# Kernel optimization log

Measured on AMD Instinct MI355X. Metric: run time of the kernel, lower is better.

Reference implementation:

```python
import jax, jax.numpy as jnp
import numpy as np

NV, NE, NI, D = 100000, 20000, 600000, 128

def setup_inputs() -> dict:
    key = jax.random.key(0)
    ks = jax.random.split(key, 16)
    inp = {
        'vfeat': jax.random.normal(ks[0], (NV, D), jnp.float32),
        'efeat': jax.random.normal(ks[1], (NE, D), jnp.float32),
        # positive regularization weights/sums (HNHN degree-based normalizers)
        'v_reg_weight': jax.random.uniform(ks[2], (NV, 1), jnp.float32, 0.5, 1.5),
        'v_reg_sum': jax.random.uniform(ks[3], (NV, 1), jnp.float32, 0.5, 1.5),
        'e_reg_weight': jax.random.uniform(ks[4], (NE, 1), jnp.float32, 0.5, 1.5),
        'e_reg_sum': jax.random.uniform(ks[5], (NE, 1), jnp.float32, 0.5, 1.5),
        'node_idx': jax.random.randint(ks[6], (NI,), 0, NV),
        'hedge_idx': jax.random.randint(ks[7], (NI,), 0, NE),
    }
    s = 1.0 / np.sqrt(D)
    inp['W1'] = jax.random.uniform(ks[8], (D, D), jnp.float32, -s, s)
    inp['b1'] = jax.random.uniform(ks[9], (D,), jnp.float32, -s, s)
    inp['Wve'] = jax.random.uniform(ks[10], (D, D), jnp.float32, -s, s)
    inp['bve'] = jax.random.uniform(ks[11], (D,), jnp.float32, -s, s)
    inp['Wev'] = jax.random.uniform(ks[12], (D, D), jnp.float32, -s, s)
    inp['bev'] = jax.random.uniform(ks[13], (D,), jnp.float32, -s, s)
    return inp


def reference(vfeat, efeat, v_reg_weight, v_reg_sum, e_reg_weight, e_reg_sum,
              node_idx, hedge_idx, W1, b1, Wve, bve, Wev, bev):
    # vertex projection (vtx_lin_1layer)
    feat_v = vfeat @ W1.T + b1                      # [NV, Dv]
    # node -> hyperedge pass ('in' etype)
    Wh_n = feat_v @ Wve.T + bve                     # [NV, De]
    w_in = v_reg_weight[node_idx] / e_reg_sum[hedge_idx]   # [NI, 1]
    feat_e = jax.ops.segment_sum(w_in * Wh_n[node_idx], hedge_idx,
                                 num_segments=NE)   # [NE, De]
    # hyperedge -> node pass ('con' etype)
    Wh_e = feat_e @ Wev.T + bev                     # [NE, Dv]
    w_con = e_reg_weight[hedge_idx] / v_reg_sum[node_idx]  # [NI, 1]
    feat_v_out = jax.ops.segment_sum(w_con * Wh_e[hedge_idx], node_idx,
                                     num_segments=NV)  # [NV, Dv]
    return feat_v_out
```

## Files before the change

### kernel.cpp

```cpp
#include <hip/hip_runtime.h>

#define D 128
#define GEMM_BLOCKS 512
#define PADE 16

typedef unsigned short ushort_t;
typedef short short8 __attribute__((ext_vector_type(8)));
typedef ushort_t ushort8v __attribute__((ext_vector_type(8)));
typedef float f32x4 __attribute__((ext_vector_type(4)));

static __device__ __forceinline__ unsigned short f2bf(float f){
  unsigned int b = __float_as_uint(f);
  unsigned int r = (b + 0x7FFFu + ((b >> 16) & 1u)) >> 16;
  return (unsigned short)r;
}
static __device__ __forceinline__ float bf2f(unsigned short u){
  return __uint_as_float(((unsigned int)u) << 16);
}


__global__ void k_wprep(const float* __restrict__ W1, const float* __restrict__ Wve,
                        const float* __restrict__ b1, const float* __restrict__ bve,
                        const float* __restrict__ Wev,
                        ushort_t* __restrict__ Wc, float* __restrict__ bc,
                        ushort_t* __restrict__ Wevb){
  int t = threadIdx.x;
  if (blockIdx.x < 128){
    int r = blockIdx.x;
    if (t < D){
      float acc = 0.f;
      for (int k = 0; k < D; ++k)
        acc += Wve[r * D + k] * W1[k * D + t];
      Wc[r * D + t] = f2bf(acc);
      if (t == 0){
        float s = 0.f;
        for (int k = 0; k < D; ++k) s += Wve[r * D + k] * b1[k];
        bc[r] = s + bve[r];
      }
    }
  } else {
    int i = (blockIdx.x - 128) * 256 + t;
    if (i < D * D) Wevb[i] = f2bf(Wev[i]);
  }
}


template<bool BF16IN>
__device__ __forceinline__ void gemm_body(const void* __restrict__ A_,
                                          const ushort_t* __restrict__ Wb,
                                          const float* __restrict__ bias,
                                          ushort_t* __restrict__ out, int M,
                                          int bid, int nblocks, ushort_t* Al){
  const int t = threadIdx.x;
  const int w = t >> 6;
  const int l = t & 63;
  const int l15 = l & 15;
  const int lh = l >> 4;

  short8 breg[4][8];
#pragma unroll
  for (int kc = 0; kc < 4; ++kc)
#pragma unroll
    for (int n0 = 0; n0 < 8; ++n0)
      breg[kc][n0] = *(const short8*)&Wb[(n0 * 16 + l15) * D + kc * 32 + lh * 8];

  float bias_r[8];
#pragma unroll
  for (int n0 = 0; n0 < 8; ++n0) bias_r[n0] = bias[n0 * 16 + l15];

  const int r_st = t >> 2;
  const int q_st = t & 3;
  const int ntile = (M + 63) >> 6;

  for (int tile = bid; tile < ntile; tile += nblocks){
    const int row0 = tile << 6;
    __syncthreads();
    {
      int r = row0 + r_st;
      ushort8v h[4];
      if (r < M){
        if (BF16IN){
          const ushort8v* src = (const ushort8v*)((const ushort_t*)A_ + (size_t)r * D + q_st * 32);
#pragma unroll
          for (int c = 0; c < 4; ++c) h[c] = src[c];
        } else {
          const float4* src = (const float4*)((const float*)A_ + (size_t)r * D + q_st * 32);
          float4 v[8];
#pragma unroll
          for (int i = 0; i < 8; ++i) v[i] = src[i];
#pragma unroll
          for (int c = 0; c < 4; ++c){
            h[c][0] = f2bf(v[2*c].x);   h[c][1] = f2bf(v[2*c].y);
            h[c][2] = f2bf(v[2*c].z);   h[c][3] = f2bf(v[2*c].w);
            h[c][4] = f2bf(v[2*c+1].x); h[c][5] = f2bf(v[2*c+1].y);
            h[c][6] = f2bf(v[2*c+1].z); h[c][7] = f2bf(v[2*c+1].w);
          }
        }
      } else {
#pragma unroll
        for (int c = 0; c < 4; ++c) h[c] = (ushort8v){0,0,0,0,0,0,0,0};
      }
#pragma unroll
      for (int c = 0; c < 4; ++c){
        int col = q_st * 32 + c * 8;
        int swz = col ^ ((r_st & 7) << 3);
        *(ushort8v*)&Al[r_st * D + swz] = h[c];
      }
    }
    __syncthreads();

    f32x4 acc[8];
#pragma unroll
    for (int n0 = 0; n0 < 8; ++n0) acc[n0] = (f32x4){0.f, 0.f, 0.f, 0.f};

#pragma unroll
    for (int kc = 0; kc < 4; ++kc){
      const int arow = w * 16 + l15;
      const int acol = (kc * 32 + lh * 8) ^ ((l15 & 7) << 3);
      short8 a = *(const short8*)&Al[arow * D + acol];
#pragma unroll
      for (int n0 = 0; n0 < 8; ++n0)
        acc[n0] = __builtin_amdgcn_mfma_f32_16x16x32_bf16(a, breg[kc][n0], acc[n0], 0, 0, 0);
    }

    const int rbase = row0 + w * 16 + lh * 4;
#pragma unroll
    for (int n0 = 0; n0 < 8; ++n0){
      const int colo = n0 * 16 + l15;
#pragma unroll
      for (int rg = 0; rg < 4; ++rg){
        int row = rbase + rg;
        if (row < M) out[(size_t)row * D + colo] = f2bf(acc[n0][rg] + bias_r[n0]);
      }
    }
  }
}

template<bool BF16IN>
__global__ __launch_bounds__(256, 2)
void k_gemm(const void* __restrict__ A_, const ushort_t* __restrict__ Wb,
            const float* __restrict__ bias, ushort_t* __restrict__ out, int M){
  __shared__ ushort_t Al[64 * D];
  gemm_body<BF16IN>(A_, Wb, bias, out, M, blockIdx.x, gridDim.x, Al);
}


__global__ __launch_bounds__(256, 2)
void k_ua(const float* __restrict__ A, const ushort_t* __restrict__ Wb,
          const float* __restrict__ bias, ushort_t* __restrict__ out, int M,
          const int* __restrict__ hedge_idx, int ni,
          int* __restrict__ cnt_e_pad, int* __restrict__ rank_e, int gb, int total){
  __shared__ ushort_t Al[64 * D];
  int i = blockIdx.x;
  long a0 = (long)i * gb / total, a1 = (long)(i + 1) * gb / total;
  if (a1 != a0){
    gemm_body<false>(A, Wb, bias, out, M, (int)a0, gb, Al);
  } else {
    int idx = (i - (int)a0) * 256 + threadIdx.x;
    if (idx < ni)
      rank_e[idx] = atomicAdd(&cnt_e_pad[hedge_idx[idx] * PADE], 1);
  }
}


template<int STRIDE>
__global__ void k_scan_partial(const int* __restrict__ cnt, int n, int* __restrict__ bsum){
  __shared__ int s[256];
  int b = blockIdx.x, t = threadIdx.x;
  int base = b * 1024;
  int acc = 0;
  for (int j = t; j < 1024; j += 256){
    int idx = base + j;
    if (idx < n) acc += cnt[(size_t)idx * STRIDE];
  }
  s[t] = acc; __syncthreads();
  for (int o = 128; o > 0; o >>= 1){
    if (t < o) s[t] += s[t + o];
    __syncthreads();
  }
  if (t == 0) bsum[b] = s[0];
}

__global__ void k_scan_bsums(int* __restrict__ bsum, int nb){
  __shared__ int s[256];
  int t = threadIdx.x;
  int runbase = 0;
  for (int base = 0; base < nb; base += 256){
    int v = (base + t < nb) ? bsum[base + t] : 0;
    s[t] = v;
    __syncthreads();
    for (int o = 1; o < 256; o <<= 1){
      int x = (t >= o) ? s[t - o] : 0;
      __syncthreads();
      s[t] += x;
      __syncthreads();
    }
    int total = s[255];
    if (base + t < nb) bsum[base + t] = runbase + (s[t] - v);
    __syncthreads();
    runbase += total;
  }
}

template<int STRIDE>
__global__ void k_scan_final(const int* __restrict__ cnt, int n,
                             const int* __restrict__ bsum, int* __restrict__ off,
                             int* __restrict__ cout){
  __shared__ int s[256];
  int b = blockIdx.x, t = threadIdx.x;
  int base = b * 1024 + t * 4;
  int v0 = (base + 0 < n) ? cnt[(size_t)(base + 0) * STRIDE] : 0;
  int v1 = (base + 1 < n) ? cnt[(size_t)(base + 1) * STRIDE] : 0;
  int v2 = (base + 2 < n) ? cnt[(size_t)(base + 2) * STRIDE] : 0;
  int v3 = (base + 3 < n) ? cnt[(size_t)(base + 3) * STRIDE] : 0;
  int lsum = v0 + v1 + v2 + v3;
  s[t] = lsum; __syncthreads();
  for (int o = 1; o < 256; o <<= 1){
    int x = (t >= o) ? s[t - o] : 0;
    __syncthreads();
    s[t] += x;
    __syncthreads();
  }
  int excl = s[t] - lsum + bsum[b];
  if (base + 0 < n){ off[base + 0] = excl;                if (cout) cout[base + 0] = v0; }
  if (base + 1 < n){ off[base + 1] = excl + v0;           if (cout) cout[base + 1] = v1; }
  if (base + 2 < n){ off[base + 2] = excl + v0 + v1;      if (cout) cout[base + 2] = v2; }
  if (base + 3 < n){ off[base + 3] = excl + v0 + v1 + v2; if (cout) cout[base + 3] = v3; }
}


__global__ void k_ub(const int* __restrict__ node_idx, const int* __restrict__ hedge_idx,
                     const int* __restrict__ rank_e, int ni,
                     const int* __restrict__ off_e, int* __restrict__ elist_v,
                     int* __restrict__ cnt_v, int* __restrict__ rank_v){
  int i = blockIdx.x;
  int idx = (i >> 1) * 256 + threadIdx.x;
  if (idx >= ni) return;
  if (i & 1){
    rank_v[idx] = atomicAdd(&cnt_v[node_idx[idx]], 1);
  } else {
    int pe = off_e[hedge_idx[idx]] + rank_e[idx];
    __builtin_nontemporal_store(node_idx[idx], &elist_v[pe]);
  }
}


template<bool BF16OUT>
__device__ __forceinline__ void scatter_g_body(const ushort_t* __restrict__ src,
                                               const int* __restrict__ off,
                                               const int* __restrict__ cnt,
                                               const int* __restrict__ list,
                                               const float* __restrict__ wnum,
                                               const float* __restrict__ dsum,
                                               void* __restrict__ dst_, int nseg,
                                               int blk_ord){
  int tid = threadIdx.x;
  int seg = blk_ord * 16 + (tid >> 4);
  if (seg >= nseg) return;
  int l16 = tid & 15;
  int s = off[seg], n = cnt[seg];
  float inv = 1.0f / dsum[seg];

  float acc[8];
#pragma unroll
  for (int c = 0; c < 8; ++c) acc[c] = 0.f;

  int j = 0;
  for (; j + 2 <= n; j += 2){
    int r0 = list[s + j];
    int r1 = list[s + j + 1];
    float w0 = wnum[r0] * inv;
    float w1 = wnum[r1] * inv;
    ushort8v x0 = *(const ushort8v*)&src[(size_t)r0 * D + l16 * 8];
    ushort8v x1 = *(const ushort8v*)&src[(size_t)r1 * D + l16 * 8];
#pragma unroll
    for (int c = 0; c < 8; ++c) acc[c] += w0 * bf2f(x0[c]) + w1 * bf2f(x1[c]);
  }
  if (j < n){
    int r0 = list[s + j];
    float w0 = wnum[r0] * inv;
    ushort8v x0 = *(const ushort8v*)&src[(size_t)r0 * D + l16 * 8];
#pragma unroll
    for (int c = 0; c < 8; ++c) acc[c] += w0 * bf2f(x0[c]);
  }

  if (BF16OUT){
    ushort8v h;
#pragma unroll
    for (int c = 0; c < 8; ++c) h[c] = f2bf(acc[c]);
    *(ushort8v*)((ushort_t*)dst_ + (size_t)seg * D + l16 * 8) = h;
  } else {
    float* dp = (float*)dst_ + (size_t)seg * D + l16 * 8;
    float4 o0, o1;
    o0.x = acc[0]; o0.y = acc[1]; o0.z = acc[2]; o0.w = acc[3];
    o1.x = acc[4]; o1.y = acc[5]; o1.z = acc[6]; o1.w = acc[7];
    *(float4*)dp = o0;
    *(float4*)(dp + 4) = o1;
  }
}

template<bool BF16OUT>
__global__ void k_scatter_g(const ushort_t* __restrict__ src,
                            const int* __restrict__ off, const int* __restrict__ cnt,
                            const int* __restrict__ list,
                            const float* __restrict__ wnum, const float* __restrict__ dsum,
                            void* __restrict__ dst_, int nseg){
  scatter_g_body<BF16OUT>(src, off, cnt, list, wnum, dsum, dst_, nseg, blockIdx.x);
}


__global__ void k_uc(const ushort_t* __restrict__ src,
                     const int* __restrict__ off_e, const int* __restrict__ cnt_e,
                     const int* __restrict__ elist,
                     const float* __restrict__ vrw, const float* __restrict__ ers,
                     ushort_t* __restrict__ feat_e, int ne, int sb, int total,
                     const int* __restrict__ node_idx, const int* __restrict__ hedge_idx,
                     const int* __restrict__ rank_v, int ni,
                     const int* __restrict__ off_v, int* __restrict__ vlist_e){
  int i = blockIdx.x;
  long a0 = (long)i * sb / total, a1 = (long)(i + 1) * sb / total;
  if (a1 != a0){
    scatter_g_body<true>(src, off_e, cnt_e, elist, vrw, ers, feat_e, ne, (int)a0);
  } else {
    int idx = (i - (int)a0) * 256 + threadIdx.x;
    if (idx < ni){
      int pv = off_v[node_idx[idx]] + rank_v[idx];
      __builtin_nontemporal_store(hedge_idx[idx], &vlist_e[pv]);
    }
  }
}


static inline int cdiv(int a, int b){ return (a + b - 1) / b; }

extern "C" void kernel_launch(void* const* d_in, const int* in_sizes, int n_in,
                              void* d_out, int out_size, void* d_ws, size_t ws_size,
                              hipStream_t stream){
  const float* vfeat        = (const float*)d_in[0];
  const float* v_reg_weight = (const float*)d_in[2];
  const float* v_reg_sum    = (const float*)d_in[3];
  const float* e_reg_weight = (const float*)d_in[4];
  const float* e_reg_sum    = (const float*)d_in[5];
  const int*   node_idx     = (const int*)d_in[6];
  const int*   hedge_idx    = (const int*)d_in[7];
  const float* W1  = (const float*)d_in[8];
  const float* b1  = (const float*)d_in[9];
  const float* Wve = (const float*)d_in[10];
  const float* bve = (const float*)d_in[11];
  const float* Wev = (const float*)d_in[12];
  const float* bev = (const float*)d_in[13];

  const int NV = in_sizes[2];
  const int NE = in_sizes[4];
  const int NI = in_sizes[6];

  char* p = (char*)d_ws;
  auto alloc = [&](size_t nbytes) -> void* {
    void* q = (void*)p;
    p += (nbytes + 255) & ~(size_t)255;
    return q;
  };

  char* zstart = p;
  int* cnt_e_pad = (int*)alloc((size_t)NE * PADE * 4);
  int* cnt_v     = (int*)alloc((size_t)NV * 4);
  size_t zbytes = (size_t)(p - zstart);

  int* cnt_e  = (int*)alloc((size_t)NE * 4);
  int* off_v  = (int*)alloc((size_t)NV * 4);
  int* off_e  = (int*)alloc((size_t)NE * 4);
  int* bsum_e = (int*)alloc(1024 * 4);
  int* bsum_v = (int*)alloc(1024 * 4);
  int* rank_v = (int*)alloc((size_t)NI * 4);
  int* rank_e = (int*)alloc((size_t)NI * 4);
  int* vlist_e = (int*)alloc((size_t)NI * 4);
  int* elist_v = (int*)alloc((size_t)NI * 4);
  ushort_t* Wc   = (ushort_t*)alloc((size_t)D * D * 2);
  ushort_t* Wevb = (ushort_t*)alloc((size_t)D * D * 2);
  float* bc      = (float*)alloc((size_t)D * 4);
  ushort_t* feat_e = (ushort_t*)alloc((size_t)NE * D * 2);
  ushort_t* Wh_e   = (ushort_t*)alloc((size_t)NE * D * 2);

  ushort_t* Wh_n = (ushort_t*)d_out;

  hipMemsetAsync(zstart, 0, zbytes, stream);

  k_wprep<<<192, 256, 0, stream>>>(W1, Wve, b1, bve, Wev, Wc, bc, Wevb);

  int cb = cdiv(NI, 256);
  int ua_total = GEMM_BLOCKS + cb;
  k_ua<<<ua_total, 256, 0, stream>>>(vfeat, Wc, bc, Wh_n, NV,
                                     hedge_idx, NI, cnt_e_pad, rank_e,
                                     GEMM_BLOCKS, ua_total);

  int nbe = cdiv(NE, 1024);
  k_scan_partial<PADE><<<nbe, 256, 0, stream>>>(cnt_e_pad, NE, bsum_e);
  k_scan_bsums<<<1, 256, 0, stream>>>(bsum_e, nbe);
  k_scan_final<PADE><<<nbe, 256, 0, stream>>>(cnt_e_pad, NE, bsum_e, off_e, cnt_e);

  k_ub<<<2 * cb, 256, 0, stream>>>(node_idx, hedge_idx, rank_e, NI,
                                   off_e, elist_v, cnt_v, rank_v);

  int nbv = cdiv(NV, 1024);
  k_scan_partial<1><<<nbv, 256, 0, stream>>>(cnt_v, NV, bsum_v);
  k_scan_bsums<<<1, 256, 0, stream>>>(bsum_v, nbv);
  k_scan_final<1><<<nbv, 256, 0, stream>>>(cnt_v, NV, bsum_v, off_v, (int*)nullptr);

  int sb = cdiv(NE, 16);
  int uc_total = sb + cb;
  k_uc<<<uc_total, 256, 0, stream>>>(Wh_n, off_e, cnt_e, elist_v,
                                     v_reg_weight, e_reg_sum, feat_e, NE, sb, uc_total,
                                     node_idx, hedge_idx, rank_v, NI,
                                     off_v, vlist_e);

  k_gemm<true><<<cdiv(NE, 64), 256, 0, stream>>>(feat_e, Wevb, bev, Wh_e, NE);

  k_scatter_g<false><<<cdiv(NV, 16), 256, 0, stream>>>(Wh_e, off_v, cnt_v, vlist_e,
                                                       e_reg_weight, v_reg_sum,
                                                       d_out, NV);
}
```

Before: 203.5 us.

## Reassociate linear maps: aggregate raw vertex features, fold all weights into one GEMM

```diff
diff --git a/kernel.cpp b/kernel.cpp
--- a/kernel.cpp
+++ b/kernel.cpp
@@ -1,8 +1,8 @@
 #include <hip/hip_runtime.h>
 
 #define D 128
-#define GEMM_BLOCKS 512
 #define PADE 16
+#define PADV 4
 
 typedef unsigned short ushort_t;
 typedef short short8 __attribute__((ext_vector_type(8)));
@@ -19,159 +19,67 @@
 }
 
 
-__global__ void k_wprep(const float* __restrict__ W1, const float* __restrict__ Wve,
-                        const float* __restrict__ b1, const float* __restrict__ bve,
-                        const float* __restrict__ Wev,
-                        ushort_t* __restrict__ Wc, float* __restrict__ bc,
-                        ushort_t* __restrict__ Wevb){
+__global__ void k_u1(const float* __restrict__ W1, const float* __restrict__ Wve,
+                     const float* __restrict__ b1, const float* __restrict__ bve,
+                     float* __restrict__ Wcf, float* __restrict__ bc,
+                     const float* __restrict__ vfeat, ushort_t* __restrict__ vbf, int nvd,
+                     const int* __restrict__ node_idx, const int* __restrict__ hedge_idx, int ni,
+                     int* __restrict__ cnt_e_pad, int* __restrict__ cnt_v_pad,
+                     int* __restrict__ rank_e, int* __restrict__ rank_v,
+                     int vb, int cb){
   int t = threadIdx.x;
-  if (blockIdx.x < 128){
-    int r = blockIdx.x;
+  int i = blockIdx.x;
+  if (i < 128){
+    int r = i;
     if (t < D){
       float acc = 0.f;
-      for (int k = 0; k < D; ++k)
-        acc += Wve[r * D + k] * W1[k * D + t];
-      Wc[r * D + t] = f2bf(acc);
+      for (int k = 0; k < D; ++k) acc += Wve[r * D + k] * W1[k * D + t];
+      Wcf[r * D + t] = acc;
       if (t == 0){
         float s = 0.f;
         for (int k = 0; k < D; ++k) s += Wve[r * D + k] * b1[k];
         bc[r] = s + bve[r];
       }
     }
+    return;
+  }
+  int j = i - 128;
+  int total = vb + cb;
+  long a0 = (long)j * vb / total, a1 = (long)(j + 1) * vb / total;
+  if (a1 != a0){
+    size_t base = (size_t)a0 * 8192;
+#pragma unroll
+    for (int c = 0; c < 4; ++c){
+      size_t e8 = base + (size_t)c * 2048 + (size_t)t * 8;
+      if (e8 < (size_t)nvd){
+        float4 v0 = *(const float4*)&vfeat[e8];
+        float4 v1 = *(const float4*)&vfeat[e8 + 4];
+        ushort8v h;
+        h[0] = f2bf(v0.x); h[1] = f2bf(v0.y); h[2] = f2bf(v0.z); h[3] = f2bf(v0.w);
+        h[4] = f2bf(v1.x); h[5] = f2bf(v1.y); h[6] = f2bf(v1.z); h[7] = f2bf(v1.w);
+        *(ushort8v*)&vbf[e8] = h;
+      }
+    }
   } else {
-    int i = (blockIdx.x - 128) * 256 + t;
-    if (i < D * D) Wevb[i] = f2bf(Wev[i]);
-  }
-}
-
-
-template<bool BF16IN>
-__device__ __forceinline__ void gemm_body(const void* __restrict__ A_,
-                                          const ushort_t* __restrict__ Wb,
-                                          const float* __restrict__ bias,
-                                          ushort_t* __restrict__ out, int M,
-                                          int bid, int nblocks, ushort_t* Al){
-  const int t = threadIdx.x;
-  const int w = t >> 6;
-  const int l = t & 63;
-  const int l15 = l & 15;
-  const int lh = l >> 4;
-
-  short8 breg[4][8];
-#pragma unroll
-  for (int kc = 0; kc < 4; ++kc)
-#pragma unroll
-    for (int n0 = 0; n0 < 8; ++n0)
-      breg[kc][n0] = *(const short8*)&Wb[(n0 * 16 + l15) * D + kc * 32 + lh * 8];
-
-  float bias_r[8];
-#pragma unroll
-  for (int n0 = 0; n0 < 8; ++n0) bias_r[n0] = bias[n0 * 16 + l15];
-
-  const int r_st = t >> 2;
-  const int q_st = t & 3;
-  const int ntile = (M + 63) >> 6;
-
-  for (int tile = bid; tile < ntile; tile += nblocks){
-    const int row0 = tile << 6;
-    __syncthreads();
-    {
-      int r = row0 + r_st;
-      ushort8v h[4];
-      if (r < M){
-        if (BF16IN){
-          const ushort8v* src = (const ushort8v*)((const ushort_t*)A_ + (size_t)r * D + q_st * 32);
-#pragma unroll
-          for (int c = 0; c < 4; ++c) h[c] = src[c];
-        } else {
-          const float4* src = (const float4*)((const float*)A_ + (size_t)r * D + q_st * 32);
-          float4 v[8];
-#pragma unroll
-          for (int i = 0; i < 8; ++i) v[i] = src[i];
-#pragma unroll
-          for (int c = 0; c < 4; ++c){
-            h[c][0] = f2bf(v[2*c].x);   h[c][1] = f2bf(v[2*c].y);
-            h[c][2] = f2bf(v[2*c].z);   h[c][3] = f2bf(v[2*c].w);
-            h[c][4] = f2bf(v[2*c+1].x); h[c][5] = f2bf(v[2*c+1].y);
-            h[c][6] = f2bf(v[2*c+1].z); h[c][7] = f2bf(v[2*c+1].w);
-          }
-        }
-      } else {
-#pragma unroll
-        for (int c = 0; c < 4; ++c) h[c] = (ushort8v){0,0,0,0,0,0,0,0};
-      }
-#pragma unroll
-      for (int c = 0; c < 4; ++c){
-        int col = q_st * 32 + c * 8;
-        int swz = col ^ ((r_st & 7) << 3);
-        *(ushort8v*)&Al[r_st * D + swz] = h[c];
-      }
-    }
-    __syncthreads();
-
-    f32x4 acc[8];
-#pragma unroll
-    for (int n0 = 0; n0 < 8; ++n0) acc[n0] = (f32x4){0.f, 0.f, 0.f, 0.f};
-
-#pragma unroll
-    for (int kc = 0; kc < 4; ++kc){
-      const int arow = w * 16 + l15;
-      const int acol = (kc * 32 + lh * 8) ^ ((l15 & 7) << 3);
-      short8 a = *(const short8*)&Al[arow * D + acol];
-#pragma unroll
-      for (int n0 = 0; n0 < 8; ++n0)
-        acc[n0] = __builtin_amdgcn_mfma_f32_16x16x32_bf16(a, breg[kc][n0], acc[n0], 0, 0, 0);
-    }
-
-    const int rbase = row0 + w * 16 + lh * 4;
-#pragma unroll
-    for (int n0 = 0; n0 < 8; ++n0){
-      const int colo = n0 * 16 + l15;
-#pragma unroll
-      for (int rg = 0; rg < 4; ++rg){
-        int row = rbase + rg;
-        if (row < M) out[(size_t)row * D + colo] = f2bf(acc[n0][rg] + bias_r[n0]);
-      }
-    }
-  }
-}
-
-template<bool BF16IN>
-__global__ __launch_bounds__(256, 2)
-void k_gemm(const void* __restrict__ A_, const ushort_t* __restrict__ Wb,
-            const float* __restrict__ bias, ushort_t* __restrict__ out, int M){
-  __shared__ ushort_t Al[64 * D];
-  gemm_body<BF16IN>(A_, Wb, bias, out, M, blockIdx.x, gridDim.x, Al);
-}
-
-
-__global__ __launch_bounds__(256, 2)
-void k_ua(const float* __restrict__ A, const ushort_t* __restrict__ Wb,
-          const float* __restrict__ bias, ushort_t* __restrict__ out, int M,
-          const int* __restrict__ hedge_idx, int ni,
-          int* __restrict__ cnt_e_pad, int* __restrict__ rank_e, int gb, int total){
-  __shared__ ushort_t Al[64 * D];
-  int i = blockIdx.x;
-  long a0 = (long)i * gb / total, a1 = (long)(i + 1) * gb / total;
-  if (a1 != a0){
-    gemm_body<false>(A, Wb, bias, out, M, (int)a0, gb, Al);
-  } else {
-    int idx = (i - (int)a0) * 256 + threadIdx.x;
-    if (idx < ni)
-      rank_e[idx] = atomicAdd(&cnt_e_pad[hedge_idx[idx] * PADE], 1);
-  }
-}
-
-
-template<int STRIDE>
-__global__ void k_scan_partial(const int* __restrict__ cnt, int n, int* __restrict__ bsum){
+    int idx = (int)(j - a0) * 256 + t;
+    if (idx < ni){
+      int n = node_idx[idx], h = hedge_idx[idx];
+      rank_e[idx] = atomicAdd(&cnt_e_pad[h * PADE], 1);
+      rank_v[idx] = atomicAdd(&cnt_v_pad[n * PADV], 1);
+    }
+  }
+}
+
+
+__device__ __forceinline__ void scan_partial_body(const int* cnt, int n, int stride,
+                                                  int* bsum, int b){
   __shared__ int s[256];
-  int b = blockIdx.x, t = threadIdx.x;
+  int t = threadIdx.x;
   int base = b * 1024;
   int acc = 0;
   for (int j = t; j < 1024; j += 256){
     int idx = base + j;
-    if (idx < n) acc += cnt[(size_t)idx * STRIDE];
+    if (idx < n) acc += cnt[(size_t)idx * stride];
   }
   s[t] = acc; __syncthreads();
   for (int o = 128; o > 0; o >>= 1){
@@ -181,7 +89,14 @@
   if (t == 0) bsum[b] = s[0];
 }
 
-__global__ void k_scan_bsums(int* __restrict__ bsum, int nb){
+__global__ void k_scan_partial2(const int* __restrict__ ce, int ne, int* __restrict__ bse,
+                                const int* __restrict__ cv, int nv, int* __restrict__ bsv,
+                                int nbe){
+  if ((int)blockIdx.x < nbe) scan_partial_body(ce, ne, PADE, bse, blockIdx.x);
+  else                       scan_partial_body(cv, nv, PADV, bsv, blockIdx.x - nbe);
+}
+
+__device__ __forceinline__ void scan_bsums_body(int* bsum, int nb){
   __shared__ int s[256];
   int t = threadIdx.x;
   int runbase = 0;
@@ -202,17 +117,20 @@
   }
 }
 
-template<int STRIDE>
-__global__ void k_scan_final(const int* __restrict__ cnt, int n,
-                             const int* __restrict__ bsum, int* __restrict__ off,
-                             int* __restrict__ cout){
+__global__ void k_scan_bsums2(int* __restrict__ bse, int nbe, int* __restrict__ bsv, int nbv){
+  if (blockIdx.x == 0) scan_bsums_body(bse, nbe);
+  else                 scan_bsums_body(bsv, nbv);
+}
+
+__device__ __forceinline__ void scan_final_body(const int* cnt, int n, int stride,
+                                                const int* bsum, int* off, int* cout, int b){
   __shared__ int s[256];
-  int b = blockIdx.x, t = threadIdx.x;
+  int t = threadIdx.x;
   int base = b * 1024 + t * 4;
-  int v0 = (base + 0 < n) ? cnt[(size_t)(base + 0) * STRIDE] : 0;
-  int v1 = (base + 1 < n) ? cnt[(size_t)(base + 1) * STRIDE] : 0;
-  int v2 = (base + 2 < n) ? cnt[(size_t)(base + 2) * STRIDE] : 0;
-  int v3 = (base + 3 < n) ? cnt[(size_t)(base + 3) * STRIDE] : 0;
+  int v0 = (base + 0 < n) ? cnt[(size_t)(base + 0) * stride] : 0;
+  int v1 = (base + 1 < n) ? cnt[(size_t)(base + 1) * stride] : 0;
+  int v2 = (base + 2 < n) ? cnt[(size_t)(base + 2) * stride] : 0;
+  int v3 = (base + 3 < n) ? cnt[(size_t)(base + 3) * stride] : 0;
   int lsum = v0 + v1 + v2 + v3;
   s[t] = lsum; __syncthreads();
   for (int o = 1; o < 256; o <<= 1){
@@ -222,40 +140,214 @@
     __syncthreads();
   }
   int excl = s[t] - lsum + bsum[b];
-  if (base + 0 < n){ off[base + 0] = excl;                if (cout) cout[base + 0] = v0; }
-  if (base + 1 < n){ off[base + 1] = excl + v0;           if (cout) cout[base + 1] = v1; }
-  if (base + 2 < n){ off[base + 2] = excl + v0 + v1;      if (cout) cout[base + 2] = v2; }
-  if (base + 3 < n){ off[base + 3] = excl + v0 + v1 + v2; if (cout) cout[base + 3] = v3; }
-}
-
-
-__global__ void k_ub(const int* __restrict__ node_idx, const int* __restrict__ hedge_idx,
+  if (base + 0 < n){ off[base + 0] = excl;                cout[base + 0] = v0; }
+  if (base + 1 < n){ off[base + 1] = excl + v0;           cout[base + 1] = v1; }
+  if (base + 2 < n){ off[base + 2] = excl + v0 + v1;      cout[base + 2] = v2; }
+  if (base + 3 < n){ off[base + 3] = excl + v0 + v1 + v2; cout[base + 3] = v3; }
+}
+
+__global__ void k_scan_final2(const int* __restrict__ ce, int ne, const int* __restrict__ bse,
+                              int* __restrict__ off_e, int* __restrict__ cnt_e,
+                              const int* __restrict__ cv, int nv, const int* __restrict__ bsv,
+                              int* __restrict__ off_v, int* __restrict__ cnt_v, int nbe){
+  if ((int)blockIdx.x < nbe) scan_final_body(ce, ne, PADE, bse, off_e, cnt_e, blockIdx.x);
+  else                       scan_final_body(cv, nv, PADV, bsv, off_v, cnt_v, blockIdx.x - nbe);
+}
+
+
+__global__ void k_u2(const float* __restrict__ Wev, const float* __restrict__ Wcf,
+                     const float* __restrict__ bc,
+                     ushort_t* __restrict__ Wcc, float* __restrict__ bvec1,
+                     const int* __restrict__ node_idx, const int* __restrict__ hedge_idx,
                      const int* __restrict__ rank_e, int ni,
-                     const int* __restrict__ off_e, int* __restrict__ elist_v,
-                     int* __restrict__ cnt_v, int* __restrict__ rank_v){
+                     const int* __restrict__ off_e, int* __restrict__ elist_v){
+  int t = threadIdx.x;
   int i = blockIdx.x;
-  int idx = (i >> 1) * 256 + threadIdx.x;
-  if (idx >= ni) return;
-  if (i & 1){
-    rank_v[idx] = atomicAdd(&cnt_v[node_idx[idx]], 1);
+  if (i < 128){
+    int r = i;
+    if (t < D){
+      float acc = 0.f;
+      for (int k = 0; k < D; ++k) acc += Wev[r * D + k] * Wcf[k * D + t];
+      Wcc[r * D + t] = f2bf(acc);
+      if (t == 0){
+        float s = 0.f;
+        for (int k = 0; k < D; ++k) s += Wev[r * D + k] * bc[k];
+        bvec1[r] = s;
+      }
+    }
   } else {
-    int pe = off_e[hedge_idx[idx]] + rank_e[idx];
-    __builtin_nontemporal_store(node_idx[idx], &elist_v[pe]);
-  }
-}
-
-
-template<bool BF16OUT>
-__device__ __forceinline__ void scatter_g_body(const ushort_t* __restrict__ src,
-                                               const int* __restrict__ off,
-                                               const int* __restrict__ cnt,
-                                               const int* __restrict__ list,
-                                               const float* __restrict__ wnum,
-                                               const float* __restrict__ dsum,
-                                               void* __restrict__ dst_, int nseg,
-                                               int blk_ord){
+    int idx = (i - 128) * 256 + t;
+    if (idx < ni){
+      int pe = off_e[hedge_idx[idx]] + rank_e[idx];
+      __builtin_nontemporal_store(node_idx[idx], &elist_v[pe]);
+    }
+  }
+}
+
+
+__global__ void k_u3(const ushort_t* __restrict__ vbf,
+                     const int* __restrict__ off_e, const int* __restrict__ cnt_e,
+                     const int* __restrict__ elist,
+                     const float* __restrict__ vrw, const float* __restrict__ ers,
+                     float* __restrict__ agg, float* __restrict__ wsum,
+                     int ne, int sb, int total,
+                     const int* __restrict__ node_idx, const int* __restrict__ hedge_idx,
+                     const int* __restrict__ rank_v, int ni,
+                     const int* __restrict__ off_v, int* __restrict__ vlist_e){
+  int i = blockIdx.x;
+  long a0 = (long)i * sb / total, a1 = (long)(i + 1) * sb / total;
+  if (a1 != a0){
+    int tid = threadIdx.x;
+    int seg = (int)a0 * 16 + (tid >> 4);
+    if (seg >= ne) return;
+    int l16 = tid & 15;
+    int s = off_e[seg], n = cnt_e[seg];
+    float inv = 1.0f / ers[seg];
+
+    float acc[8];
+#pragma unroll
+    for (int c = 0; c < 8; ++c) acc[c] = 0.f;
+    float wa = 0.f;
+
+    int j = 0;
+    for (; j + 2 <= n; j += 2){
+      int r0 = elist[s + j];
+      int r1 = elist[s + j + 1];
+      float w0 = vrw[r0];
+      float w1 = vrw[r1];
+      ushort8v x0 = *(const ushort8v*)&vbf[(size_t)r0 * D + l16 * 8];
+      ushort8v x1 = *(const ushort8v*)&vbf[(size_t)r1 * D + l16 * 8];
+      wa += w0 + w1;
+#pragma unroll
+      for (int c = 0; c < 8; ++c) acc[c] += w0 * bf2f(x0[c]) + w1 * bf2f(x1[c]);
+    }
+    if (j < n){
+      int r0 = elist[s + j];
+      float w0 = vrw[r0];
+      ushort8v x0 = *(const ushort8v*)&vbf[(size_t)r0 * D + l16 * 8];
+      wa += w0;
+#pragma unroll
+      for (int c = 0; c < 8; ++c) acc[c] += w0 * bf2f(x0[c]);
+    }
+
+    float* dp = &agg[(size_t)seg * D + l16 * 8];
+    float4 o0, o1;
+    o0.x = acc[0] * inv; o0.y = acc[1] * inv; o0.z = acc[2] * inv; o0.w = acc[3] * inv;
+    o1.x = acc[4] * inv; o1.y = acc[5] * inv; o1.z = acc[6] * inv; o1.w = acc[7] * inv;
+    *(float4*)dp = o0;
+    *(float4*)(dp + 4) = o1;
+    if (l16 == 0) wsum[seg] = wa * inv;
+  } else {
+    int idx = (int)(i - a0) * 256 + threadIdx.x;
+    if (idx < ni){
+      int pv = off_v[node_idx[idx]] + rank_v[idx];
+      __builtin_nontemporal_store(hedge_idx[idx], &vlist_e[pv]);
+    }
+  }
+}
+
+
+__global__ __launch_bounds__(256, 2)
+void k_gemm_rs(const float* __restrict__ A, const ushort_t* __restrict__ Wb,
+               const float* __restrict__ wsum, const float* __restrict__ bvec1,
+               const float* __restrict__ bev, ushort_t* __restrict__ out, int M){
+  __shared__ ushort_t Al[64 * D];
+
+  const int t = threadIdx.x;
+  const int w = t >> 6;
+  const int l = t & 63;
+  const int l15 = l & 15;
+  const int lh = l >> 4;
+
+  short8 breg[4][8];
+#pragma unroll
+  for (int kc = 0; kc < 4; ++kc)
+#pragma unroll
+    for (int n0 = 0; n0 < 8; ++n0)
+      breg[kc][n0] = *(const short8*)&Wb[(n0 * 16 + l15) * D + kc * 32 + lh * 8];
+
+  float bv1_r[8], bev_r[8];
+#pragma unroll
+  for (int n0 = 0; n0 < 8; ++n0){
+    bv1_r[n0] = bvec1[n0 * 16 + l15];
+    bev_r[n0] = bev[n0 * 16 + l15];
+  }
+
+  const int r_st = t >> 2;
+  const int q_st = t & 3;
+  const int ntile = (M + 63) >> 6;
+
+  for (int tile = blockIdx.x; tile < ntile; tile += gridDim.x){
+    const int row0 = tile << 6;
+    __syncthreads();
+    {
+      int r = row0 + r_st;
+      ushort8v h[4];
+      if (r < M){
+        const float4* src = (const float4*)&A[(size_t)r * D + q_st * 32];
+        float4 v[8];
+#pragma unroll
+        for (int ii = 0; ii < 8; ++ii) v[ii] = src[ii];
+#pragma unroll
+        for (int c = 0; c < 4; ++c){
+          h[c][0] = f2bf(v[2*c].x);   h[c][1] = f2bf(v[2*c].y);
+          h[c][2] = f2bf(v[2*c].z);   h[c][3] = f2bf(v[2*c].w);
+          h[c][4] = f2bf(v[2*c+1].x); h[c][5] = f2bf(v[2*c+1].y);
+          h[c][6] = f2bf(v[2*c+1].z); h[c][7] = f2bf(v[2*c+1].w);
+        }
+      } else {
+#pragma unroll
+        for (int c = 0; c < 4; ++c) h[c] = (ushort8v){0,0,0,0,0,0,0,0};
+      }
+#pragma unroll
+      for (int c = 0; c < 4; ++c){
+        int col = q_st * 32 + c * 8;
+        int swz = col ^ ((r_st & 7) << 3);
+        *(ushort8v*)&Al[r_st * D + swz] = h[c];
+      }
+    }
+    __syncthreads();
+
+    f32x4 acc[8];
+#pragma unroll
+    for (int n0 = 0; n0 < 8; ++n0) acc[n0] = (f32x4){0.f, 0.f, 0.f, 0.f};
+
+#pragma unroll
+    for (int kc = 0; kc < 4; ++kc){
+      const int arow = w * 16 + l15;
+      const int acol = (kc * 32 + lh * 8) ^ ((l15 & 7) << 3);
+      short8 a = *(const short8*)&Al[arow * D + acol];
+#pragma unroll
+      for (int n0 = 0; n0 < 8; ++n0)
+        acc[n0] = __builtin_amdgcn_mfma_f32_16x16x32_bf16(a, breg[kc][n0], acc[n0], 0, 0, 0);
+    }
+
+    const int rbase = row0 + w * 16 + lh * 4;
+    float w4[4];
+#pragma unroll
+    for (int rg = 0; rg < 4; ++rg)
+      w4[rg] = (rbase + rg < M) ? wsum[rbase + rg] : 0.f;
+#pragma unroll
+    for (int n0 = 0; n0 < 8; ++n0){
+      const int colo = n0 * 16 + l15;
+#pragma unroll
+      for (int rg = 0; rg < 4; ++rg){
+        int row = rbase + rg;
+        if (row < M)
+          out[(size_t)row * D + colo] = f2bf(acc[n0][rg] + w4[rg] * bv1_r[n0] + bev_r[n0]);
+      }
+    }
+  }
+}
+
+
+__global__ void k_scatter2(const ushort_t* __restrict__ src,
+                           const int* __restrict__ off, const int* __restrict__ cnt,
+                           const int* __restrict__ list,
+                           const float* __restrict__ wnum, const float* __restrict__ dsum,
+                           float* __restrict__ dst, int nseg){
   int tid = threadIdx.x;
-  int seg = blk_ord * 16 + (tid >> 4);
+  int seg = blockIdx.x * 16 + (tid >> 4);
   if (seg >= nseg) return;
   int l16 = tid & 15;
   int s = off[seg], n = cnt[seg];
@@ -284,50 +376,12 @@
     for (int c = 0; c < 8; ++c) acc[c] += w0 * bf2f(x0[c]);
   }
 
-  if (BF16OUT){
-    ushort8v h;
-#pragma unroll
-    for (int c = 0; c < 8; ++c) h[c] = f2bf(acc[c]);
-    *(ushort8v*)((ushort_t*)dst_ + (size_t)seg * D + l16 * 8) = h;
-  } else {
-    float* dp = (float*)dst_ + (size_t)seg * D + l16 * 8;
-    float4 o0, o1;
-    o0.x = acc[0]; o0.y = acc[1]; o0.z = acc[2]; o0.w = acc[3];
-    o1.x = acc[4]; o1.y = acc[5]; o1.z = acc[6]; o1.w = acc[7];
-    *(float4*)dp = o0;
-    *(float4*)(dp + 4) = o1;
-  }
-}
-
-template<bool BF16OUT>
-__global__ void k_scatter_g(const ushort_t* __restrict__ src,
-                            const int* __restrict__ off, const int* __restrict__ cnt,
-                            const int* __restrict__ list,
-                            const float* __restrict__ wnum, const float* __restrict__ dsum,
-                            void* __restrict__ dst_, int nseg){
-  scatter_g_body<BF16OUT>(src, off, cnt, list, wnum, dsum, dst_, nseg, blockIdx.x);
-}
-
-
-__global__ void k_uc(const ushort_t* __restrict__ src,
-                     const int* __restrict__ off_e, const int* __restrict__ cnt_e,
-                     const int* __restrict__ elist,
-                     const float* __restrict__ vrw, const float* __restrict__ ers,
-                     ushort_t* __restrict__ feat_e, int ne, int sb, int total,
-                     const int* __restrict__ node_idx, const int* __restrict__ hedge_idx,
-                     const int* __restrict__ rank_v, int ni,
-                     const int* __restrict__ off_v, int* __restrict__ vlist_e){
-  int i = blockIdx.x;
-  long a0 = (long)i * sb / total, a1 = (long)(i + 1) * sb / total;
-  if (a1 != a0){
-    scatter_g_body<true>(src, off_e, cnt_e, elist, vrw, ers, feat_e, ne, (int)a0);
-  } else {
-    int idx = (i - (int)a0) * 256 + threadIdx.x;
-    if (idx < ni){
-      int pv = off_v[node_idx[idx]] + rank_v[idx];
-      __builtin_nontemporal_store(hedge_idx[idx], &vlist_e[pv]);
-    }
-  }
+  float* dp = &dst[(size_t)seg * D + l16 * 8];
+  float4 o0, o1;
+  o0.x = acc[0]; o0.y = acc[1]; o0.z = acc[2]; o0.w = acc[3];
+  o1.x = acc[4]; o1.y = acc[5]; o1.z = acc[6]; o1.w = acc[7];
+  *(float4*)dp = o0;
+  *(float4*)(dp + 4) = o1;
 }
 
 
@@ -353,6 +407,7 @@
   const int NV = in_sizes[2];
   const int NE = in_sizes[4];
   const int NI = in_sizes[6];
+  const int NVD = NV * D;
 
   char* p = (char*)d_ws;
   auto alloc = [&](size_t nbytes) -> void* {
@@ -363,59 +418,61 @@
 
   char* zstart = p;
   int* cnt_e_pad = (int*)alloc((size_t)NE * PADE * 4);
-  int* cnt_v     = (int*)alloc((size_t)NV * 4);
+  int* cnt_v_pad = (int*)alloc((size_t)NV * PADV * 4);
   size_t zbytes = (size_t)(p - zstart);
 
   int* cnt_e  = (int*)alloc((size_t)NE * 4);
+  int* cnt_v  = (int*)alloc((size_t)NV * 4);
+  int* off_e  = (int*)alloc((size_t)NE * 4);
   int* off_v  = (int*)alloc((size_t)NV * 4);
-  int* off_e  = (int*)alloc((size_t)NE * 4);
   int* bsum_e = (int*)alloc(1024 * 4);
   int* bsum_v = (int*)alloc(1024 * 4);
+  int* rank_e = (int*)alloc((size_t)NI * 4);
   int* rank_v = (int*)alloc((size_t)NI * 4);
-  int* rank_e = (int*)alloc((size_t)NI * 4);
+  int* elist_v = (int*)alloc((size_t)NI * 4);
   int* vlist_e = (int*)alloc((size_t)NI * 4);
-  int* elist_v = (int*)alloc((size_t)NI * 4);
-  ushort_t* Wc   = (ushort_t*)alloc((size_t)D * D * 2);
-  ushort_t* Wevb = (ushort_t*)alloc((size_t)D * D * 2);
+  float* Wcf     = (float*)alloc((size_t)D * D * 4);
   float* bc      = (float*)alloc((size_t)D * 4);
-  ushort_t* feat_e = (ushort_t*)alloc((size_t)NE * D * 2);
-  ushort_t* Wh_e   = (ushort_t*)alloc((size_t)NE * D * 2);
-
-  ushort_t* Wh_n = (ushort_t*)d_out;
+  ushort_t* Wcc  = (ushort_t*)alloc((size_t)D * D * 2);
+  float* bvec1   = (float*)alloc((size_t)D * 4);
+  ushort_t* Wh_e = (ushort_t*)alloc((size_t)NE * D * 2);
+
+  ushort_t* vbf  = (ushort_t*)d_out;
+  float*    agg  = (float*)((char*)d_out + (size_t)NVD * 2);
+  float*    wsum = (float*)((char*)d_out + (size_t)NVD * 2 + (size_t)NE * D * 4);
 
   hipMemsetAsync(zstart, 0, zbytes, stream);
 
-  k_wprep<<<192, 256, 0, stream>>>(W1, Wve, b1, bve, Wev, Wc, bc, Wevb);
-
   int cb = cdiv(NI, 256);
-  int ua_total = GEMM_BLOCKS + cb;
-  k_ua<<<ua_total, 256, 0, stream>>>(vfeat, Wc, bc, Wh_n, NV,
-                                     hedge_idx, NI, cnt_e_pad, rank_e,
-                                     GEMM_BLOCKS, ua_total);
-
-  int nbe = cdiv(NE, 1024);
-  k_scan_partial<PADE><<<nbe, 256, 0, stream>>>(cnt_e_pad, NE, bsum_e);
-  k_scan_bsums<<<1, 256, 0, stream>>>(bsum_e, nbe);
-  k_scan_final<PADE><<<nbe, 256, 0, stream>>>(cnt_e_pad, NE, bsum_e, off_e, cnt_e);
-
-  k_ub<<<2 * cb, 256, 0, stream>>>(node_idx, hedge_idx, rank_e, NI,
-                                   off_e, elist_v, cnt_v, rank_v);
-
-  int nbv = cdiv(NV, 1024);
-  k_scan_partial<1><<<nbv, 256, 0, stream>>>(cnt_v, NV, bsum_v);
-  k_scan_bsums<<<1, 256, 0, stream>>>(bsum_v, nbv);
-  k_scan_final<1><<<nbv, 256, 0, stream>>>(cnt_v, NV, bsum_v, off_v, (int*)nullptr);
+  int vb = cdiv(NVD, 8192);
+  k_u1<<<128 + vb + cb, 256, 0, stream>>>(W1, Wve, b1, bve, Wcf, bc,
+                                          vfeat, vbf, NVD,
+                                          node_idx, hedge_idx, NI,
+                                          cnt_e_pad, cnt_v_pad, rank_e, rank_v,
+                                          vb, cb);
+
+  int nbe = cdiv(NE, 1024), nbv = cdiv(NV, 1024);
+  k_scan_partial2<<<nbe + nbv, 256, 0, stream>>>(cnt_e_pad, NE, bsum_e,
+                                                 cnt_v_pad, NV, bsum_v, nbe);
+  k_scan_bsums2<<<2, 256, 0, stream>>>(bsum_e, nbe, bsum_v, nbv);
+  k_scan_final2<<<nbe + nbv, 256, 0, stream>>>(cnt_e_pad, NE, bsum_e, off_e, cnt_e,
+                                               cnt_v_pad, NV, bsum_v, off_v, cnt_v, nbe);
+
+  k_u2<<<128 + cb, 256, 0, stream>>>(Wev, Wcf, bc, Wcc, bvec1,
+                                     node_idx, hedge_idx, rank_e, NI,
+                                     off_e, elist_v);
 
   int sb = cdiv(NE, 16);
-  int uc_total = sb + cb;
-  k_uc<<<uc_total, 256, 0, stream>>>(Wh_n, off_e, cnt_e, elist_v,
-                                     v_reg_weight, e_reg_sum, feat_e, NE, sb, uc_total,
+  int u3_total = sb + cb;
+  k_u3<<<u3_total, 256, 0, stream>>>(vbf, off_e, cnt_e, elist_v,
+                                     v_reg_weight, e_reg_sum,
+                                     agg, wsum, NE, sb, u3_total,
                                      node_idx, hedge_idx, rank_v, NI,
                                      off_v, vlist_e);
 
-  k_gemm<true><<<cdiv(NE, 64), 256, 0, stream>>>(feat_e, Wevb, bev, Wh_e, NE);
-
-  k_scatter_g<false><<<cdiv(NV, 16), 256, 0, stream>>>(Wh_e, off_v, cnt_v, vlist_e,
-                                                       e_reg_weight, v_reg_sum,
-                                                       d_out, NV);
-}
+  k_gemm_rs<<<cdiv(NE, 64), 256, 0, stream>>>(agg, Wcc, wsum, bvec1, bev, Wh_e, NE);
+
+  k_scatter2<<<cdiv(NV, 16), 256, 0, stream>>>(Wh_e, off_v, cnt_v, vlist_e,
+                                               e_reg_weight, v_reg_sum,
+                                               (float*)d_out, NV);
+}
```

Result: faster. 179.7 us (-11.7%).
